# Kernel tuning notes

Measured on AMD Instinct MI355X. Metric: run time of the kernel, lower is better.

Reference implementation:

```python
import jax, jax.numpy as jnp
import numpy as np

EMBED = 512
OUT_DIM = 512
BS = 512


def _linear(x, W, b):
    return x @ W + b


def setup_inputs() -> dict:
    key = jax.random.key(0)
    ks = jax.random.split(key, 12)
    s = 1.0 / np.sqrt(EMBED)
    inp = {
        "image_features": jax.random.normal(ks[0], (BS, EMBED), jnp.float32),
        "text_features": jax.random.normal(ks[1], (BS, EMBED), jnp.float32),
        "cell_id": 1,
        # fusion weights (stored [in, out])
        "Wx": jax.random.uniform(ks[2], (EMBED, EMBED), jnp.float32, -s, s),
        "bx": jax.random.uniform(ks[3], (EMBED,), jnp.float32, -s, s),
        "Wy": jax.random.uniform(ks[4], (EMBED, EMBED), jnp.float32, -s, s),
        "by": jax.random.uniform(ks[5], (EMBED,), jnp.float32, -s, s),
        "Wo": jax.random.uniform(ks[6], (EMBED, OUT_DIM), jnp.float32, -s, s),
        "bo": jax.random.uniform(ks[7], (OUT_DIM,), jnp.float32, -s, s),
        # attention MLP weights
        "Wa1": jax.random.uniform(ks[8], (EMBED, EMBED), jnp.float32, -s, s),
        "ba1": jax.random.uniform(ks[9], (EMBED,), jnp.float32, -s, s),
        "Wa2": jax.random.uniform(ks[10], (EMBED, EMBED), jnp.float32, -s, s),
        "ba2": jax.random.uniform(ks[11], (EMBED,), jnp.float32, -s, s),
    }
    return inp


def reference(image_features, text_features, cell_id, Wx, bx, Wy, by, Wo, bo, Wa1, ba1, Wa2, ba2):
    # AttentionMechanism: Linear -> ReLU -> Linear -> Softmax over feature dim (dim=1)
    h = jax.nn.relu(_linear(text_features, Wa1, ba1))
    attn = jax.nn.softmax(_linear(h, Wa2, ba2), axis=1)
    text = attn * text_features  # [bs, d]

    out_x = _linear(image_features, Wx, bx)          # [bs, d]
    gate = jax.nn.sigmoid(_linear(text, Wy, by))     # [bs, d]

    if cell_id != 0 and cell_id != 3:
        # outs[i, j] = fc_out(gate[i] * out_x[j])  -> [bs, bs, out_dim]
        prod = gate[:, None, :] * out_x[None, :, :]  # [bs, bs, d]
        return jnp.einsum('ijd,do->ijo', prod, Wo) + bo
    else:
        return _linear(gate * out_x, Wo, bo)
```

## Files before the change

kernel.cpp:

```cpp
#include <hip/hip_runtime.h>
#include <hip/hip_bf16.h>

typedef __attribute__((ext_vector_type(4))) float f32x4;
typedef __attribute__((ext_vector_type(8))) __bf16 bf16x8;

__device__ __forceinline__ void gld_lds16(const void* g, void* l) {
  __builtin_amdgcn_global_load_lds((__attribute__((address_space(1))) void*)(g),
                                   (__attribute__((address_space(3))) void*)(l),
                                   16, 0, 0);
}

__device__ __forceinline__ f32x4 mfma16(bf16x8 a, bf16x8 b, f32x4 c) {
  return __builtin_amdgcn_mfma_f32_16x16x32_bf16(a, b, c, 0, 0, 0);
}

__device__ __forceinline__ bf16x8 cvt8(f32x4 a, f32x4 b) {
  bf16x8 r;
  r[0] = (__bf16)a.x; r[1] = (__bf16)a.y; r[2] = (__bf16)a.z; r[3] = (__bf16)a.w;
  r[4] = (__bf16)b.x; r[5] = (__bf16)b.y; r[6] = (__bf16)b.z; r[7] = (__bf16)b.w;
  return r;
}

__device__ __forceinline__ bf16x8 mulcvt8(f32x4 a, f32x4 b, f32x4 g0, f32x4 g1) {
  bf16x8 r;
  r[0] = (__bf16)(a.x * g0.x); r[1] = (__bf16)(a.y * g0.y);
  r[2] = (__bf16)(a.z * g0.z); r[3] = (__bf16)(a.w * g0.w);
  r[4] = (__bf16)(b.x * g1.x); r[5] = (__bf16)(b.y * g1.y);
  r[6] = (__bf16)(b.z * g1.z); r[7] = (__bf16)(b.w * g1.w);
  return r;
}

struct P5 {
  const float* s[5];
  __bf16* d[5];
};

__global__ __launch_bounds__(256) void transpose_cvt_k(P5 p) {
  __shared__ __bf16 tile[64][66];
  const float* src = p.s[blockIdx.z];
  __bf16* dst = p.d[blockIdx.z];
  const int x = threadIdx.x & 63, y = threadIdx.x >> 6;
  const int n0 = blockIdx.x * 64, k0 = blockIdx.y * 64;
#pragma unroll
  for (int r = 0; r < 16; ++r) {
    int k = r * 4 + y;
    tile[k][x] = (__bf16)src[(size_t)(k0 + k) * 512 + n0 + x];
  }
  __syncthreads();
#pragma unroll
  for (int r = 0; r < 16; ++r) {
    int n = r * 4 + y;
    dst[(size_t)(n0 + n) * 512 + k0 + x] = tile[x][n];
  }
}

template <int ACT>
__global__ __launch_bounds__(256) void gemm512(const float* __restrict__ A,
                                               const __bf16* __restrict__ Bt,
                                               const float* __restrict__ bias,
                                               float* __restrict__ C) {
  __shared__ alignas(16) __bf16 Als[64 * 32];
  __shared__ alignas(16) __bf16 Bls[64 * 32];
  const int t = threadIdx.x;
  const int w = t >> 6, L = t & 63, lq = L >> 4, l16 = L & 15;
  const int m0 = (blockIdx.x & 7) * 64, n0 = (blockIdx.x >> 3) * 64;
  const int wm = (w & 1) * 32, wn = (w >> 1) * 32;
  const int row = t >> 2, p = t & 3;
  const int q = p ^ ((row >> 1) & 3);

  const float* ap = A + (size_t)(m0 + row) * 512 + q * 8;
  const __bf16* bp = Bt + (size_t)(n0 + row) * 512 + q * 8;
  __bf16* aw = &Als[row * 32 + p * 8];
  void* bl = (void*)&Bls[w * 512];
  const int sq8 = (lq ^ ((l16 >> 1) & 3)) * 8;

  const f32x4 fz = {0.f, 0.f, 0.f, 0.f};
  f32x4 acc[2][2] = {{fz, fz}, {fz, fz}};

  for (int kt = 0; kt < 16; ++kt) {
    const int k0 = kt * 32;
    if (kt) __syncthreads();
    f32x4 a0 = *(const f32x4*)(ap + k0);
    f32x4 a1 = *(const f32x4*)(ap + k0 + 4);
    *(bf16x8*)aw = cvt8(a0, a1);
    gld_lds16(bp + k0, bl);
    __syncthreads();
    bf16x8 af[2], bb[2];
#pragma unroll
    for (int mt = 0; mt < 2; ++mt)
      af[mt] = *(const bf16x8*)&Als[(wm + mt * 16 + l16) * 32 + sq8];
#pragma unroll
    for (int nt = 0; nt < 2; ++nt)
      bb[nt] = *(const bf16x8*)&Bls[(wn + nt * 16 + l16) * 32 + sq8];
#pragma unroll
    for (int mt = 0; mt < 2; ++mt)
#pragma unroll
      for (int nt = 0; nt < 2; ++nt)
        acc[mt][nt] = mfma16(af[mt], bb[nt], acc[mt][nt]);
  }

#pragma unroll
  for (int nt = 0; nt < 2; ++nt) {
    const int o = n0 + wn + nt * 16 + l16;
    const float bv = bias[o];
#pragma unroll
    for (int mt = 0; mt < 2; ++mt) {
      const int mb = m0 + wm + mt * 16 + lq * 4;
#pragma unroll
      for (int r = 0; r < 4; ++r) {
        float v = acc[mt][nt][r] + bv;
        if (ACT == 1) v = fmaxf(v, 0.f);
        if (ACT == 2) v = 1.0f / (1.0f + __expf(-v));
        C[(size_t)(mb + r) * 512 + o] = v;
      }
    }
  }
}

__global__ __launch_bounds__(256) void softmax_mul_k(const float* __restrict__ S,
                                                     const float* __restrict__ T,
                                                     float* __restrict__ O) {
  const int i = blockIdx.x, t = threadIdx.x, w = t >> 6, L = t & 63;
  __shared__ float red[8];
  float v0 = S[i * 512 + t];
  float v1 = S[i * 512 + 256 + t];
  float m = fmaxf(v0, v1);
  for (int off = 32; off; off >>= 1) m = fmaxf(m, __shfl_xor(m, off));
  if (L == 0) red[w] = m;
  __syncthreads();
  m = fmaxf(fmaxf(red[0], red[1]), fmaxf(red[2], red[3]));
  float e0 = __expf(v0 - m), e1 = __expf(v1 - m);
  float sm = e0 + e1;
  for (int off = 32; off; off >>= 1) sm += __shfl_xor(sm, off);
  if (L == 0) red[4 + w] = sm;
  __syncthreads();
  sm = (red[4] + red[5]) + (red[6] + red[7]);
  const float inv = 1.0f / sm;
  O[i * 512 + t] = e0 * inv * T[i * 512 + t];
  O[i * 512 + 256 + t] = e1 * inv * T[i * 512 + 256 + t];
}

__global__ __launch_bounds__(256, 3) void einsum_main(
    const float* __restrict__ OX, const float* __restrict__ GATE,
    const __bf16* __restrict__ WOT, const float* __restrict__ BO,
    float* __restrict__ OUT) {
  __shared__ alignas(16) __bf16 Als[128 * 32];
  __shared__ alignas(16) __bf16 Bls[128 * 32];
  const int t = threadIdx.x;
  const int bx = blockIdx.x;
  const int i = bx >> 4;
  const int j0 = ((bx >> 2) & 3) * 128;
  const int o0 = (bx & 3) * 128;
  const int w = t >> 6, L = t & 63, lq = L >> 4, l16 = L & 15;
  const int wm = (w & 1) * 64, wn = (w >> 1) * 64;
  const int r0 = t >> 2, p = t & 3;
  const int q = p ^ ((r0 >> 1) & 3);

  const float* ox0 = OX + (size_t)(j0 + r0) * 512 + q * 8;
  const float* ox1 = ox0 + (size_t)64 * 512;
  const float* gp = GATE + (size_t)i * 512 + q * 8;
  const __bf16* wo0 = WOT + (size_t)(o0 + r0) * 512 + q * 8;
  const __bf16* wo1 = wo0 + (size_t)64 * 512;
  __bf16* aw0 = &Als[r0 * 32 + p * 8];
  __bf16* aw1 = &Als[(r0 + 64) * 32 + p * 8];
  void* bl0 = (void*)&Bls[w * 512];
  void* bl1 = (void*)&Bls[(w + 4) * 512];
  const int sq8 = (lq ^ ((l16 >> 1) & 3)) * 8;

  const f32x4 fz = {0.f, 0.f, 0.f, 0.f};
  f32x4 acc[4][4];
#pragma unroll
  for (int a = 0; a < 4; ++a)
#pragma unroll
    for (int b = 0; b < 4; ++b) acc[a][b] = fz;

  f32x4 xa0 = *(const f32x4*)ox0, xa1 = *(const f32x4*)(ox0 + 4);
  f32x4 xb0 = *(const f32x4*)ox1, xb1 = *(const f32x4*)(ox1 + 4);
  f32x4 g0 = *(const f32x4*)gp, g1 = *(const f32x4*)(gp + 4);

  for (int kt = 0; kt < 16; ++kt) {
    const int k0 = kt * 32;
    if (kt) __syncthreads();
    *(bf16x8*)aw0 = mulcvt8(xa0, xa1, g0, g1);
    *(bf16x8*)aw1 = mulcvt8(xb0, xb1, g0, g1);
    gld_lds16(wo0 + k0, bl0);
    gld_lds16(wo1 + k0, bl1);
    __syncthreads();
    if (kt < 15) {
      xa0 = *(const f32x4*)(ox0 + k0 + 32);
      xa1 = *(const f32x4*)(ox0 + k0 + 36);
      xb0 = *(const f32x4*)(ox1 + k0 + 32);
      xb1 = *(const f32x4*)(ox1 + k0 + 36);
      g0 = *(const f32x4*)(gp + k0 + 32);
      g1 = *(const f32x4*)(gp + k0 + 36);
    }
    bf16x8 af[4], bb[4];
#pragma unroll
    for (int mt = 0; mt < 4; ++mt)
      af[mt] = *(const bf16x8*)&Als[(wm + mt * 16 + l16) * 32 + sq8];
#pragma unroll
    for (int nt = 0; nt < 4; ++nt)
      bb[nt] = *(const bf16x8*)&Bls[(wn + nt * 16 + l16) * 32 + sq8];
#pragma unroll
    for (int mt = 0; mt < 4; ++mt)
#pragma unroll
      for (int nt = 0; nt < 4; ++nt)
        acc[mt][nt] = mfma16(af[mt], bb[nt], acc[mt][nt]);
  }

  const size_t obase = (size_t)i * 512 * 512;
#pragma unroll
  for (int nt = 0; nt < 4; ++nt) {
    const int o = o0 + wn + nt * 16 + l16;
    const float bv = BO[o];
#pragma unroll
    for (int mt = 0; mt < 4; ++mt) {
      const int jb = j0 + wm + mt * 16 + lq * 4;
#pragma unroll
      for (int r = 0; r < 4; ++r)
        OUT[obase + (size_t)(jb + r) * 512 + o] = acc[mt][nt][r] + bv;
    }
  }
}

extern "C" void kernel_launch(void* const* d_in, const int* in_sizes, int n_in,
                              void* d_out, int out_size, void* d_ws, size_t ws_size,
                              hipStream_t stream) {
  (void)in_sizes; (void)n_in; (void)out_size; (void)ws_size;
  const float* image = (const float*)d_in[0];
  const float* text  = (const float*)d_in[1];
  const float* Wx  = (const float*)d_in[3];
  const float* bx  = (const float*)d_in[4];
  const float* Wy  = (const float*)d_in[5];
  const float* by  = (const float*)d_in[6];
  const float* Wo  = (const float*)d_in[7];
  const float* bo  = (const float*)d_in[8];
  const float* Wa1 = (const float*)d_in[9];
  const float* ba1 = (const float*)d_in[10];
  const float* Wa2 = (const float*)d_in[11];
  const float* ba2 = (const float*)d_in[12];

  char* ws = (char*)d_ws;
  const size_t HB = 512 * 1024;
  const size_t FB = 1024 * 1024;
  __bf16* tWx  = (__bf16*)(ws + 0 * HB);
  __bf16* tWy  = (__bf16*)(ws + 1 * HB);
  __bf16* tWo  = (__bf16*)(ws + 2 * HB);
  __bf16* tWa1 = (__bf16*)(ws + 3 * HB);
  __bf16* tWa2 = (__bf16*)(ws + 4 * HB);
  char* fb = ws + 5 * HB;
  float* hbuf  = (float*)(fb + 0 * FB);
  float* sbuf  = (float*)(fb + 1 * FB);
  float* t2    = (float*)(fb + 2 * FB);
  float* oxb   = (float*)(fb + 3 * FB);
  float* gateb = (float*)(fb + 4 * FB);

  P5 p;
  p.s[0] = Wx;  p.d[0] = tWx;
  p.s[1] = Wy;  p.d[1] = tWy;
  p.s[2] = Wo;  p.d[2] = tWo;
  p.s[3] = Wa1; p.d[3] = tWa1;
  p.s[4] = Wa2; p.d[4] = tWa2;
  transpose_cvt_k<<<dim3(8, 8, 5), 256, 0, stream>>>(p);

  gemm512<1><<<64, 256, 0, stream>>>(text, tWa1, ba1, hbuf);
  gemm512<0><<<64, 256, 0, stream>>>(hbuf, tWa2, ba2, sbuf);
  softmax_mul_k<<<512, 256, 0, stream>>>(sbuf, text, t2);
  gemm512<0><<<64, 256, 0, stream>>>(image, tWx, bx, oxb);
  gemm512<2><<<64, 256, 0, stream>>>(t2, tWy, by, gateb);
  einsum_main<<<8192, 256, 0, stream>>>(oxb, gateb, tWo, bo, (float*)d_out);
}
```

Before: 728.7 us.

## Materialize gated bf16 products and batch independent small GEMMs

Independent GEMMs (Wa1 and Wx) are merged into one launch via blockIdx.y. If the workspace is large enough, the einsum no longer does an on-the-fly multiply and convert. A prescale kernel instead writes the full 512x512x512 bf16 gate*out_x tensor (256 MB), and a plain GEMM then streams it into LDS with direct global-to-LDS loads, using a swizzled block order. This trades the in-loop conversion work for a large extra memory write and read, and it only runs when ws_size allows.

```diff
diff --git a/kernel.cpp b/kernel.cpp
--- a/kernel.cpp
+++ b/kernel.cpp
@@ -54,16 +54,25 @@
   }
 }
 
-template <int ACT>
-__global__ __launch_bounds__(256) void gemm512(const float* __restrict__ A,
-                                               const __bf16* __restrict__ Bt,
-                                               const float* __restrict__ bias,
-                                               float* __restrict__ C) {
+struct GemmArgs {
+  const float* A;
+  const __bf16* Bt;
+  const float* bias;
+  float* C;
+  int act;
+};
+struct GemmPair { GemmArgs g[2]; };
+
+__device__ __forceinline__ void gemm512_body(const float* __restrict__ A,
+                                             const __bf16* __restrict__ Bt,
+                                             const float* __restrict__ bias,
+                                             float* __restrict__ C, int act,
+                                             int bidx) {
   __shared__ alignas(16) __bf16 Als[64 * 32];
   __shared__ alignas(16) __bf16 Bls[64 * 32];
   const int t = threadIdx.x;
   const int w = t >> 6, L = t & 63, lq = L >> 4, l16 = L & 15;
-  const int m0 = (blockIdx.x & 7) * 64, n0 = (blockIdx.x >> 3) * 64;
+  const int m0 = (bidx & 7) * 64, n0 = (bidx >> 3) * 64;
   const int wm = (w & 1) * 32, wn = (w >> 1) * 32;
   const int row = t >> 2, p = t & 3;
   const int q = p ^ ((row >> 1) & 3);
@@ -109,12 +118,21 @@
 #pragma unroll
       for (int r = 0; r < 4; ++r) {
         float v = acc[mt][nt][r] + bv;
-        if (ACT == 1) v = fmaxf(v, 0.f);
-        if (ACT == 2) v = 1.0f / (1.0f + __expf(-v));
+        if (act == 1) v = fmaxf(v, 0.f);
+        else if (act == 2) v = 1.0f / (1.0f + __expf(-v));
         C[(size_t)(mb + r) * 512 + o] = v;
       }
     }
   }
+}
+
+__global__ __launch_bounds__(256) void gemm512_one(GemmArgs a) {
+  gemm512_body(a.A, a.Bt, a.bias, a.C, a.act, blockIdx.x);
+}
+
+__global__ __launch_bounds__(256) void gemm512_two(GemmPair p) {
+  GemmArgs a = p.g[blockIdx.y];
+  gemm512_body(a.A, a.Bt, a.bias, a.C, a.act, blockIdx.x);
 }
 
 __global__ __launch_bounds__(256) void softmax_mul_k(const float* __restrict__ S,
@@ -140,6 +158,90 @@
   O[i * 512 + 256 + t] = e1 * inv * T[i * 512 + 256 + t];
 }
 
+__global__ __launch_bounds__(256) void prescale_k(const float* __restrict__ OX,
+                                                  const float* __restrict__ GATE,
+                                                  __bf16* __restrict__ A) {
+  const int total = 512 * 512 * 64;
+  const int stride = gridDim.x * 256;
+  for (int c = blockIdx.x * 256 + threadIdx.x; c < total; c += stride) {
+    const int d8 = c & 63, j = (c >> 6) & 511, i = c >> 15;
+    const float* ox = OX + j * 512 + d8 * 8;
+    const float* gp = GATE + i * 512 + d8 * 8;
+    f32x4 x0 = *(const f32x4*)ox, x1 = *(const f32x4*)(ox + 4);
+    f32x4 g0 = *(const f32x4*)gp, g1 = *(const f32x4*)(gp + 4);
+    *(bf16x8*)(A + (size_t)c * 8) = mulcvt8(x0, x1, g0, g1);
+  }
+}
+
+__global__ __launch_bounds__(256, 3) void einsum_gemm(
+    const __bf16* __restrict__ Aall, const __bf16* __restrict__ WOT,
+    const float* __restrict__ BO, float* __restrict__ OUT) {
+  __shared__ alignas(16) __bf16 Als[128 * 32];
+  __shared__ alignas(16) __bf16 Bls[128 * 32];
+  const int t = threadIdx.x;
+  const int bx = (blockIdx.x & 7) * 1024 + (blockIdx.x >> 3);
+  const int i = bx >> 4;
+  const int j0 = ((bx >> 2) & 3) * 128;
+  const int o0 = (bx & 3) * 128;
+  const int w = t >> 6, L = t & 63, lq = L >> 4, l16 = L & 15;
+  const int wm = (w & 1) * 64, wn = (w >> 1) * 64;
+  const int r0 = t >> 2, p = t & 3;
+  const int q = p ^ ((r0 >> 1) & 3);
+
+  const __bf16* a0 = Aall + ((size_t)i * 512 + j0 + r0) * 512 + q * 8;
+  const __bf16* a1 = a0 + (size_t)64 * 512;
+  const __bf16* b0 = WOT + (size_t)(o0 + r0) * 512 + q * 8;
+  const __bf16* b1 = b0 + (size_t)64 * 512;
+  void* al0 = (void*)&Als[w * 512];
+  void* al1 = (void*)&Als[(w + 4) * 512];
+  void* bl0 = (void*)&Bls[w * 512];
+  void* bl1 = (void*)&Bls[(w + 4) * 512];
+  const int sq8 = (lq ^ ((l16 >> 1) & 3)) * 8;
+
+  const f32x4 fz = {0.f, 0.f, 0.f, 0.f};
+  f32x4 acc[4][4];
+#pragma unroll
+  for (int a = 0; a < 4; ++a)
+#pragma unroll
+    for (int b = 0; b < 4; ++b) acc[a][b] = fz;
+
+  for (int kt = 0; kt < 16; ++kt) {
+    const int k0 = kt * 32;
+    if (kt) __syncthreads();
+    gld_lds16(a0 + k0, al0);
+    gld_lds16(a1 + k0, al1);
+    gld_lds16(b0 + k0, bl0);
+    gld_lds16(b1 + k0, bl1);
+    __syncthreads();
+    bf16x8 af[4], bb[4];
+#pragma unroll
+    for (int mt = 0; mt < 4; ++mt)
+      af[mt] = *(const bf16x8*)&Als[(wm + mt * 16 + l16) * 32 + sq8];
+#pragma unroll
+    for (int nt = 0; nt < 4; ++nt)
+      bb[nt] = *(const bf16x8*)&Bls[(wn + nt * 16 + l16) * 32 + sq8];
+#pragma unroll
+    for (int mt = 0; mt < 4; ++mt)
+#pragma unroll
+      for (int nt = 0; nt < 4; ++nt)
+        acc[mt][nt] = mfma16(af[mt], bb[nt], acc[mt][nt]);
+  }
+
+  const size_t obase = (size_t)i * 512 * 512;
+#pragma unroll
+  for (int nt = 0; nt < 4; ++nt) {
+    const int o = o0 + wn + nt * 16 + l16;
+    const float bv = BO[o];
+#pragma unroll
+    for (int mt = 0; mt < 4; ++mt) {
+      const int jb = j0 + wm + mt * 16 + lq * 4;
+#pragma unroll
+      for (int r = 0; r < 4; ++r)
+        OUT[obase + (size_t)(jb + r) * 512 + o] = acc[mt][nt][r] + bv;
+    }
+  }
+}
+
 __global__ __launch_bounds__(256, 3) void einsum_main(
     const float* __restrict__ OX, const float* __restrict__ GATE,
     const __bf16* __restrict__ WOT, const float* __restrict__ BO,
@@ -226,7 +328,7 @@
 extern "C" void kernel_launch(void* const* d_in, const int* in_sizes, int n_in,
                               void* d_out, int out_size, void* d_ws, size_t ws_size,
                               hipStream_t stream) {
-  (void)in_sizes; (void)n_in; (void)out_size; (void)ws_size;
+  (void)in_sizes; (void)n_in; (void)out_size;
   const float* image = (const float*)d_in[0];
   const float* text  = (const float*)d_in[1];
   const float* Wx  = (const float*)d_in[3];
@@ -254,6 +356,9 @@
   float* t2    = (float*)(fb + 2 * FB);
   float* oxb   = (float*)(fb + 3 * FB);
   float* gateb = (float*)(fb + 4 * FB);
+  __bf16* Aall = (__bf16*)(fb + 5 * FB);
+  const size_t need_big =
+      5 * HB + 5 * FB + (size_t)512 * 512 * 512 * 2;
 
   P5 p;
   p.s[0] = Wx;  p.d[0] = tWx;
@@ -263,10 +368,18 @@
   p.s[4] = Wa2; p.d[4] = tWa2;
   transpose_cvt_k<<<dim3(8, 8, 5), 256, 0, stream>>>(p);
 
-  gemm512<1><<<64, 256, 0, stream>>>(text, tWa1, ba1, hbuf);
-  gemm512<0><<<64, 256, 0, stream>>>(hbuf, tWa2, ba2, sbuf);
+  GemmPair pp;
+  pp.g[0] = GemmArgs{text, tWa1, ba1, hbuf, 1};
+  pp.g[1] = GemmArgs{image, tWx, bx, oxb, 0};
+  gemm512_two<<<dim3(64, 2), 256, 0, stream>>>(pp);
+  gemm512_one<<<64, 256, 0, stream>>>(GemmArgs{hbuf, tWa2, ba2, sbuf, 0});
   softmax_mul_k<<<512, 256, 0, stream>>>(sbuf, text, t2);
-  gemm512<0><<<64, 256, 0, stream>>>(image, tWx, bx, oxb);
-  gemm512<2><<<64, 256, 0, stream>>>(t2, tWy, by, gateb);
-  einsum_main<<<8192, 256, 0, stream>>>(oxb, gateb, tWo, bo, (float*)d_out);
-}
+  gemm512_one<<<64, 256, 0, stream>>>(GemmArgs{t2, tWy, by, gateb, 2});
+
+  if (ws_size >= need_big) {
+    prescale_k<<<4096, 256, 0, stream>>>(oxb, gateb, Aall);
+    einsum_gemm<<<8192, 256, 0, stream>>>(Aall, tWo, bo, (float*)d_out);
+  } else {
+    einsum_main<<<8192, 256, 0, stream>>>(oxb, gateb, tWo, bo, (float*)d_out);
+  }
+}
```

Result: slower. 785.3 us (+7.8%).

## Rework einsum kernel tiling with K=64 stages, 8 waves, and vectorized stores

Applied to the files above, without the earlier changes.

The main einsum kernel now runs 512 threads (8 waves) per 128x128 tile with a 64-wide K step and an XOR swizzle over 8 chunks. It swaps the MFMA operand order so each lane holds 4 consecutive output columns and can write them with one float4 store. The image projection GEMM is also batched into one launch with the first attention GEMM to cut launch count. The aim is fewer barriers, wider coalesced writes of the large output, and better latency hiding, at the cost of more LDS per block and lower per-wave reuse.

```diff
diff --git a/kernel.cpp b/kernel.cpp
--- a/kernel.cpp
+++ b/kernel.cpp
@@ -54,16 +54,25 @@
   }
 }
 
-template <int ACT>
-__global__ __launch_bounds__(256) void gemm512(const float* __restrict__ A,
-                                               const __bf16* __restrict__ Bt,
-                                               const float* __restrict__ bias,
-                                               float* __restrict__ C) {
+struct GemmArgs {
+  const float* A;
+  const __bf16* Bt;
+  const float* bias;
+  float* C;
+  int act;
+};
+struct GemmPair { GemmArgs g[2]; };
+
+__device__ __forceinline__ void gemm512_body(const float* __restrict__ A,
+                                             const __bf16* __restrict__ Bt,
+                                             const float* __restrict__ bias,
+                                             float* __restrict__ C, int act,
+                                             int bidx) {
   __shared__ alignas(16) __bf16 Als[64 * 32];
   __shared__ alignas(16) __bf16 Bls[64 * 32];
   const int t = threadIdx.x;
   const int w = t >> 6, L = t & 63, lq = L >> 4, l16 = L & 15;
-  const int m0 = (blockIdx.x & 7) * 64, n0 = (blockIdx.x >> 3) * 64;
+  const int m0 = (bidx & 7) * 64, n0 = (bidx >> 3) * 64;
   const int wm = (w & 1) * 32, wn = (w >> 1) * 32;
   const int row = t >> 2, p = t & 3;
   const int q = p ^ ((row >> 1) & 3);
@@ -109,12 +118,21 @@
 #pragma unroll
       for (int r = 0; r < 4; ++r) {
         float v = acc[mt][nt][r] + bv;
-        if (ACT == 1) v = fmaxf(v, 0.f);
-        if (ACT == 2) v = 1.0f / (1.0f + __expf(-v));
+        if (act == 1) v = fmaxf(v, 0.f);
+        else if (act == 2) v = 1.0f / (1.0f + __expf(-v));
         C[(size_t)(mb + r) * 512 + o] = v;
       }
     }
   }
+}
+
+__global__ __launch_bounds__(256) void gemm512_one(GemmArgs a) {
+  gemm512_body(a.A, a.Bt, a.bias, a.C, a.act, blockIdx.x);
+}
+
+__global__ __launch_bounds__(256) void gemm512_two(GemmPair p) {
+  GemmArgs a = p.g[blockIdx.y];
+  gemm512_body(a.A, a.Bt, a.bias, a.C, a.act, blockIdx.x);
 }
 
 __global__ __launch_bounds__(256) void softmax_mul_k(const float* __restrict__ S,
@@ -140,85 +158,110 @@
   O[i * 512 + 256 + t] = e1 * inv * T[i * 512 + 256 + t];
 }
 
-__global__ __launch_bounds__(256, 3) void einsum_main(
+__global__ __launch_bounds__(512, 4) void einsum_v2(
     const float* __restrict__ OX, const float* __restrict__ GATE,
     const __bf16* __restrict__ WOT, const float* __restrict__ BO,
     float* __restrict__ OUT) {
-  __shared__ alignas(16) __bf16 Als[128 * 32];
-  __shared__ alignas(16) __bf16 Bls[128 * 32];
+  __shared__ alignas(16) __bf16 Als[128 * 64];
+  __shared__ alignas(16) __bf16 Bls[128 * 64];
   const int t = threadIdx.x;
   const int bx = blockIdx.x;
   const int i = bx >> 4;
   const int j0 = ((bx >> 2) & 3) * 128;
   const int o0 = (bx & 3) * 128;
   const int w = t >> 6, L = t & 63, lq = L >> 4, l16 = L & 15;
-  const int wm = (w & 1) * 64, wn = (w >> 1) * 64;
-  const int r0 = t >> 2, p = t & 3;
-  const int q = p ^ ((r0 >> 1) & 3);
-
-  const float* ox0 = OX + (size_t)(j0 + r0) * 512 + q * 8;
-  const float* ox1 = ox0 + (size_t)64 * 512;
-  const float* gp = GATE + (size_t)i * 512 + q * 8;
-  const __bf16* wo0 = WOT + (size_t)(o0 + r0) * 512 + q * 8;
-  const __bf16* wo1 = wo0 + (size_t)64 * 512;
-  __bf16* aw0 = &Als[r0 * 32 + p * 8];
-  __bf16* aw1 = &Als[(r0 + 64) * 32 + p * 8];
+  const int wj = (w & 1) * 64;
+  const int wo = (w >> 1) * 32;
+
+  const int rA = t >> 2;
+  const int lc0 = (t & 3) * 2, lc1 = lc0 + 1;
+  __bf16* aw0 = &Als[rA * 64 + ((lc0 ^ (rA & 7)) * 8)];
+  __bf16* aw1 = &Als[rA * 64 + ((lc1 ^ (rA & 7)) * 8)];
+  const float* oxp = OX + (size_t)(j0 + rA) * 512;
+  const float* gp = GATE + (size_t)i * 512;
+  const int oo0 = lc0 * 8, oo1 = lc1 * 8;
+
+  const int rB = t >> 3;
+  const int qB = (t & 7) ^ (rB & 7);
+  const __bf16* bsrc0 = WOT + (size_t)(o0 + rB) * 512 + qB * 8;
+  const __bf16* bsrc1 = WOT + (size_t)(o0 + 64 + rB) * 512 + qB * 8;
   void* bl0 = (void*)&Bls[w * 512];
-  void* bl1 = (void*)&Bls[(w + 4) * 512];
-  const int sq8 = (lq ^ ((l16 >> 1) & 3)) * 8;
+  void* bl1 = (void*)&Bls[4096 + w * 512];
+
+  const int cx0 = ((lq ^ (l16 & 7)) * 8);
+  const int cx1 = (((4 + lq) ^ (l16 & 7)) * 8);
+  const int arow = (wj + l16) * 64;
+  const int brow = (wo + l16) * 64;
 
   const f32x4 fz = {0.f, 0.f, 0.f, 0.f};
-  f32x4 acc[4][4];
+  f32x4 acc[4][2];
 #pragma unroll
   for (int a = 0; a < 4; ++a)
 #pragma unroll
-    for (int b = 0; b < 4; ++b) acc[a][b] = fz;
-
-  f32x4 xa0 = *(const f32x4*)ox0, xa1 = *(const f32x4*)(ox0 + 4);
-  f32x4 xb0 = *(const f32x4*)ox1, xb1 = *(const f32x4*)(ox1 + 4);
-  f32x4 g0 = *(const f32x4*)gp, g1 = *(const f32x4*)(gp + 4);
-
-  for (int kt = 0; kt < 16; ++kt) {
-    const int k0 = kt * 32;
+    for (int b = 0; b < 2; ++b) acc[a][b] = fz;
+
+  f32x4 x0a = *(const f32x4*)(oxp + oo0);
+  f32x4 x0b = *(const f32x4*)(oxp + oo0 + 4);
+  f32x4 x1a = *(const f32x4*)(oxp + oo1);
+  f32x4 x1b = *(const f32x4*)(oxp + oo1 + 4);
+  f32x4 g0a = *(const f32x4*)(gp + oo0);
+  f32x4 g0b = *(const f32x4*)(gp + oo0 + 4);
+  f32x4 g1a = *(const f32x4*)(gp + oo1);
+  f32x4 g1b = *(const f32x4*)(gp + oo1 + 4);
+
+  for (int kt = 0; kt < 8; ++kt) {
+    const int k0 = kt * 64;
     if (kt) __syncthreads();
-    *(bf16x8*)aw0 = mulcvt8(xa0, xa1, g0, g1);
-    *(bf16x8*)aw1 = mulcvt8(xb0, xb1, g0, g1);
-    gld_lds16(wo0 + k0, bl0);
-    gld_lds16(wo1 + k0, bl1);
+    *(bf16x8*)aw0 = mulcvt8(x0a, x0b, g0a, g0b);
+    *(bf16x8*)aw1 = mulcvt8(x1a, x1b, g1a, g1b);
+    gld_lds16(bsrc0 + k0, bl0);
+    gld_lds16(bsrc1 + k0, bl1);
     __syncthreads();
-    if (kt < 15) {
-      xa0 = *(const f32x4*)(ox0 + k0 + 32);
-      xa1 = *(const f32x4*)(ox0 + k0 + 36);
-      xb0 = *(const f32x4*)(ox1 + k0 + 32);
-      xb1 = *(const f32x4*)(ox1 + k0 + 36);
-      g0 = *(const f32x4*)(gp + k0 + 32);
-      g1 = *(const f32x4*)(gp + k0 + 36);
+    if (kt < 7) {
+      x0a = *(const f32x4*)(oxp + k0 + 64 + oo0);
+      x0b = *(const f32x4*)(oxp + k0 + 64 + oo0 + 4);
+      x1a = *(const f32x4*)(oxp + k0 + 64 + oo1);
+      x1b = *(const f32x4*)(oxp + k0 + 64 + oo1 + 4);
+      g0a = *(const f32x4*)(gp + k0 + 64 + oo0);
+      g0b = *(const f32x4*)(gp + k0 + 64 + oo0 + 4);
+      g1a = *(const f32x4*)(gp + k0 + 64 + oo1);
+      g1b = *(const f32x4*)(gp + k0 + 64 + oo1 + 4);
     }
-    bf16x8 af[4], bb[4];
+    bf16x8 af[4], bb[2];
 #pragma unroll
     for (int mt = 0; mt < 4; ++mt)
-      af[mt] = *(const bf16x8*)&Als[(wm + mt * 16 + l16) * 32 + sq8];
-#pragma unroll
-    for (int nt = 0; nt < 4; ++nt)
-      bb[nt] = *(const bf16x8*)&Bls[(wn + nt * 16 + l16) * 32 + sq8];
+      af[mt] = *(const bf16x8*)&Als[arow + mt * 1024 + cx0];
+#pragma unroll
+    for (int nt = 0; nt < 2; ++nt)
+      bb[nt] = *(const bf16x8*)&Bls[brow + nt * 1024 + cx0];
 #pragma unroll
     for (int mt = 0; mt < 4; ++mt)
 #pragma unroll
-      for (int nt = 0; nt < 4; ++nt)
-        acc[mt][nt] = mfma16(af[mt], bb[nt], acc[mt][nt]);
+      for (int nt = 0; nt < 2; ++nt)
+        acc[mt][nt] = mfma16(bb[nt], af[mt], acc[mt][nt]);
+#pragma unroll
+    for (int mt = 0; mt < 4; ++mt)
+      af[mt] = *(const bf16x8*)&Als[arow + mt * 1024 + cx1];
+#pragma unroll
+    for (int nt = 0; nt < 2; ++nt)
+      bb[nt] = *(const bf16x8*)&Bls[brow + nt * 1024 + cx1];
+#pragma unroll
+    for (int mt = 0; mt < 4; ++mt)
+#pragma unroll
+      for (int nt = 0; nt < 2; ++nt)
+        acc[mt][nt] = mfma16(bb[nt], af[mt], acc[mt][nt]);
   }
 
   const size_t obase = (size_t)i * 512 * 512;
 #pragma unroll
-  for (int nt = 0; nt < 4; ++nt) {
-    const int o = o0 + wn + nt * 16 + l16;
-    const float bv = BO[o];
+  for (int nt = 0; nt < 2; ++nt) {
+    const int ob = o0 + wo + nt * 16 + lq * 4;
+    const f32x4 bo4 = *(const f32x4*)(BO + ob);
 #pragma unroll
     for (int mt = 0; mt < 4; ++mt) {
-      const int jb = j0 + wm + mt * 16 + lq * 4;
-#pragma unroll
-      for (int r = 0; r < 4; ++r)
-        OUT[obase + (size_t)(jb + r) * 512 + o] = acc[mt][nt][r] + bv;
+      const int j = j0 + wj + mt * 16 + l16;
+      f32x4 v = acc[mt][nt] + bo4;
+      *(f32x4*)(OUT + obase + (size_t)j * 512 + ob) = v;
     }
   }
 }
@@ -263,10 +306,12 @@
   p.s[4] = Wa2; p.d[4] = tWa2;
   transpose_cvt_k<<<dim3(8, 8, 5), 256, 0, stream>>>(p);
 
-  gemm512<1><<<64, 256, 0, stream>>>(text, tWa1, ba1, hbuf);
-  gemm512<0><<<64, 256, 0, stream>>>(hbuf, tWa2, ba2, sbuf);
+  GemmPair pp;
+  pp.g[0] = GemmArgs{text, tWa1, ba1, hbuf, 1};
+  pp.g[1] = GemmArgs{image, tWx, bx, oxb, 0};
+  gemm512_two<<<dim3(64, 2), 256, 0, stream>>>(pp);
+  gemm512_one<<<64, 256, 0, stream>>>(GemmArgs{hbuf, tWa2, ba2, sbuf, 0});
   softmax_mul_k<<<512, 256, 0, stream>>>(sbuf, text, t2);
-  gemm512<0><<<64, 256, 0, stream>>>(image, tWx, bx, oxb);
-  gemm512<2><<<64, 256, 0, stream>>>(t2, tWy, by, gateb);
-  einsum_main<<<8192, 256, 0, stream>>>(oxb, gateb, tWo, bo, (float*)d_out);
-}
+  gemm512_one<<<64, 256, 0, stream>>>(GemmArgs{t2, tWy, by, gateb, 2});
+  einsum_v2<<<8192, 512, 0, stream>>>(oxb, gateb, tWo, bo, (float*)d_out);
+}
```

Measured after the change: 846.1 us. +16.1%, slower.

## Double-buffer einsum LDS tiles, loop 4 gate rows per block, batch independent GEMMs

Applied to the files above, without the earlier changes.

The main einsum kernel now double-buffers its A and B tiles in LDS and prefetches the next two stages into registers. This leaves one barrier per k-step and overlaps loads with MFMA work. Each block now handles 4 consecutive i rows, reusing the same OX/Wo tile indices, which cuts the grid from 8192 to 2048 blocks. The two independent small GEMMs (Wa1 and Wx) are merged into one launch via blockIdx.y, trading compile-time activation templates for a runtime flag. Doubling LDS use may lower occupancy.

```diff
diff --git a/kernel.cpp b/kernel.cpp
--- a/kernel.cpp
+++ b/kernel.cpp
@@ -54,16 +54,25 @@
   }
 }
 
-template <int ACT>
-__global__ __launch_bounds__(256) void gemm512(const float* __restrict__ A,
-                                               const __bf16* __restrict__ Bt,
-                                               const float* __restrict__ bias,
-                                               float* __restrict__ C) {
+struct GemmArgs {
+  const float* A;
+  const __bf16* Bt;
+  const float* bias;
+  float* C;
+  int act;
+};
+struct GemmPair { GemmArgs g[2]; };
+
+__device__ __forceinline__ void gemm512_body(const float* __restrict__ A,
+                                             const __bf16* __restrict__ Bt,
+                                             const float* __restrict__ bias,
+                                             float* __restrict__ C, int act,
+                                             int bidx) {
   __shared__ alignas(16) __bf16 Als[64 * 32];
   __shared__ alignas(16) __bf16 Bls[64 * 32];
   const int t = threadIdx.x;
   const int w = t >> 6, L = t & 63, lq = L >> 4, l16 = L & 15;
-  const int m0 = (blockIdx.x & 7) * 64, n0 = (blockIdx.x >> 3) * 64;
+  const int m0 = (bidx & 7) * 64, n0 = (bidx >> 3) * 64;
   const int wm = (w & 1) * 32, wn = (w >> 1) * 32;
   const int row = t >> 2, p = t & 3;
   const int q = p ^ ((row >> 1) & 3);
@@ -109,12 +118,21 @@
 #pragma unroll
       for (int r = 0; r < 4; ++r) {
         float v = acc[mt][nt][r] + bv;
-        if (ACT == 1) v = fmaxf(v, 0.f);
-        if (ACT == 2) v = 1.0f / (1.0f + __expf(-v));
+        if (act == 1) v = fmaxf(v, 0.f);
+        else if (act == 2) v = 1.0f / (1.0f + __expf(-v));
         C[(size_t)(mb + r) * 512 + o] = v;
       }
     }
   }
+}
+
+__global__ __launch_bounds__(256) void gemm512_one(GemmArgs a) {
+  gemm512_body(a.A, a.Bt, a.bias, a.C, a.act, blockIdx.x);
+}
+
+__global__ __launch_bounds__(256) void gemm512_two(GemmPair p) {
+  GemmArgs a = p.g[blockIdx.y];
+  gemm512_body(a.A, a.Bt, a.bias, a.C, a.act, blockIdx.x);
 }
 
 __global__ __launch_bounds__(256) void softmax_mul_k(const float* __restrict__ S,
@@ -140,15 +158,28 @@
   O[i * 512 + 256 + t] = e1 * inv * T[i * 512 + 256 + t];
 }
 
-__global__ __launch_bounds__(256, 3) void einsum_main(
+struct AStage {
+  f32x4 xa0, xa1, xb0, xb1, g0, g1;
+};
+
+__device__ __forceinline__ AStage load_stage(const float* ox0, const float* ox1,
+                                             const float* gp, int k0) {
+  AStage s;
+  s.xa0 = *(const f32x4*)(ox0 + k0); s.xa1 = *(const f32x4*)(ox0 + k0 + 4);
+  s.xb0 = *(const f32x4*)(ox1 + k0); s.xb1 = *(const f32x4*)(ox1 + k0 + 4);
+  s.g0  = *(const f32x4*)(gp + k0);  s.g1  = *(const f32x4*)(gp + k0 + 4);
+  return s;
+}
+
+__global__ __launch_bounds__(256, 3) void einsum_v3(
     const float* __restrict__ OX, const float* __restrict__ GATE,
     const __bf16* __restrict__ WOT, const float* __restrict__ BO,
     float* __restrict__ OUT) {
-  __shared__ alignas(16) __bf16 Als[128 * 32];
-  __shared__ alignas(16) __bf16 Bls[128 * 32];
+  __shared__ alignas(16) __bf16 Als[2][128 * 32];
+  __shared__ alignas(16) __bf16 Bls[2][128 * 32];
   const int t = threadIdx.x;
   const int bx = blockIdx.x;
-  const int i = bx >> 4;
+  const int i0 = (bx >> 4) * 4;
   const int j0 = ((bx >> 2) & 3) * 128;
   const int o0 = (bx & 3) * 128;
   const int w = t >> 6, L = t & 63, lq = L >> 4, l16 = L & 15;
@@ -158,67 +189,70 @@
 
   const float* ox0 = OX + (size_t)(j0 + r0) * 512 + q * 8;
   const float* ox1 = ox0 + (size_t)64 * 512;
-  const float* gp = GATE + (size_t)i * 512 + q * 8;
   const __bf16* wo0 = WOT + (size_t)(o0 + r0) * 512 + q * 8;
   const __bf16* wo1 = wo0 + (size_t)64 * 512;
-  __bf16* aw0 = &Als[r0 * 32 + p * 8];
-  __bf16* aw1 = &Als[(r0 + 64) * 32 + p * 8];
-  void* bl0 = (void*)&Bls[w * 512];
-  void* bl1 = (void*)&Bls[(w + 4) * 512];
+  const int awo = r0 * 32 + p * 8;
   const int sq8 = (lq ^ ((l16 >> 1) & 3)) * 8;
 
-  const f32x4 fz = {0.f, 0.f, 0.f, 0.f};
-  f32x4 acc[4][4];
-#pragma unroll
-  for (int a = 0; a < 4; ++a)
-#pragma unroll
-    for (int b = 0; b < 4; ++b) acc[a][b] = fz;
-
-  f32x4 xa0 = *(const f32x4*)ox0, xa1 = *(const f32x4*)(ox0 + 4);
-  f32x4 xb0 = *(const f32x4*)ox1, xb1 = *(const f32x4*)(ox1 + 4);
-  f32x4 g0 = *(const f32x4*)gp, g1 = *(const f32x4*)(gp + 4);
-
-  for (int kt = 0; kt < 16; ++kt) {
-    const int k0 = kt * 32;
-    if (kt) __syncthreads();
-    *(bf16x8*)aw0 = mulcvt8(xa0, xa1, g0, g1);
-    *(bf16x8*)aw1 = mulcvt8(xb0, xb1, g0, g1);
-    gld_lds16(wo0 + k0, bl0);
-    gld_lds16(wo1 + k0, bl1);
+  for (int g = 0; g < 4; ++g) {
+    const float* gp = GATE + (size_t)(i0 + g) * 512 + q * 8;
+
+    const f32x4 fz = {0.f, 0.f, 0.f, 0.f};
+    f32x4 acc[4][4];
+#pragma unroll
+    for (int a = 0; a < 4; ++a)
+#pragma unroll
+      for (int b = 0; b < 4; ++b) acc[a][b] = fz;
+
+    AStage S[2];
+    S[0] = load_stage(ox0, ox1, gp, 0);
+    *(bf16x8*)&Als[0][awo] = mulcvt8(S[0].xa0, S[0].xa1, S[0].g0, S[0].g1);
+    *(bf16x8*)&Als[0][awo + 64 * 32] =
+        mulcvt8(S[0].xb0, S[0].xb1, S[0].g0, S[0].g1);
+    gld_lds16(wo0, (void*)&Bls[0][w * 512]);
+    gld_lds16(wo1, (void*)&Bls[0][(w + 4) * 512]);
+    S[1] = load_stage(ox0, ox1, gp, 32);
     __syncthreads();
-    if (kt < 15) {
-      xa0 = *(const f32x4*)(ox0 + k0 + 32);
-      xa1 = *(const f32x4*)(ox0 + k0 + 36);
-      xb0 = *(const f32x4*)(ox1 + k0 + 32);
-      xb1 = *(const f32x4*)(ox1 + k0 + 36);
-      g0 = *(const f32x4*)(gp + k0 + 32);
-      g1 = *(const f32x4*)(gp + k0 + 36);
+
+#pragma unroll
+    for (int kt = 0; kt < 16; ++kt) {
+      const int cb = kt & 1, nb = cb ^ 1;
+      if (kt < 15) {
+        *(bf16x8*)&Als[nb][awo] =
+            mulcvt8(S[nb].xa0, S[nb].xa1, S[nb].g0, S[nb].g1);
+        *(bf16x8*)&Als[nb][awo + 64 * 32] =
+            mulcvt8(S[nb].xb0, S[nb].xb1, S[nb].g0, S[nb].g1);
+        gld_lds16(wo0 + (kt + 1) * 32, (void*)&Bls[nb][w * 512]);
+        gld_lds16(wo1 + (kt + 1) * 32, (void*)&Bls[nb][(w + 4) * 512]);
+      }
+      if (kt < 14) S[cb] = load_stage(ox0, ox1, gp, (kt + 2) * 32);
+      bf16x8 af[4], bb[4];
+#pragma unroll
+      for (int mt = 0; mt < 4; ++mt)
+        af[mt] = *(const bf16x8*)&Als[cb][(wm + mt * 16 + l16) * 32 + sq8];
+#pragma unroll
+      for (int nt = 0; nt < 4; ++nt)
+        bb[nt] = *(const bf16x8*)&Bls[cb][(wn + nt * 16 + l16) * 32 + sq8];
+#pragma unroll
+      for (int mt = 0; mt < 4; ++mt)
+#pragma unroll
+        for (int nt = 0; nt < 4; ++nt)
+          acc[mt][nt] = mfma16(af[mt], bb[nt], acc[mt][nt]);
+      __syncthreads();
     }
-    bf16x8 af[4], bb[4];
-#pragma unroll
-    for (int mt = 0; mt < 4; ++mt)
-      af[mt] = *(const bf16x8*)&Als[(wm + mt * 16 + l16) * 32 + sq8];
-#pragma unroll
-    for (int nt = 0; nt < 4; ++nt)
-      bb[nt] = *(const bf16x8*)&Bls[(wn + nt * 16 + l16) * 32 + sq8];
-#pragma unroll
-    for (int mt = 0; mt < 4; ++mt)
-#pragma unroll
-      for (int nt = 0; nt < 4; ++nt)
-        acc[mt][nt] = mfma16(af[mt], bb[nt], acc[mt][nt]);
-  }
-
-  const size_t obase = (size_t)i * 512 * 512;
-#pragma unroll
-  for (int nt = 0; nt < 4; ++nt) {
-    const int o = o0 + wn + nt * 16 + l16;
-    const float bv = BO[o];
-#pragma unroll
-    for (int mt = 0; mt < 4; ++mt) {
-      const int jb = j0 + wm + mt * 16 + lq * 4;
-#pragma unroll
-      for (int r = 0; r < 4; ++r)
-        OUT[obase + (size_t)(jb + r) * 512 + o] = acc[mt][nt][r] + bv;
+
+    const size_t obase = (size_t)(i0 + g) * 512 * 512;
+#pragma unroll
+    for (int nt = 0; nt < 4; ++nt) {
+      const int o = o0 + wn + nt * 16 + l16;
+      const float bv = BO[o];
+#pragma unroll
+      for (int mt = 0; mt < 4; ++mt) {
+        const int jb = j0 + wm + mt * 16 + lq * 4;
+#pragma unroll
+        for (int r = 0; r < 4; ++r)
+          OUT[obase + (size_t)(jb + r) * 512 + o] = acc[mt][nt][r] + bv;
+      }
     }
   }
 }
@@ -263,10 +297,12 @@
   p.s[4] = Wa2; p.d[4] = tWa2;
   transpose_cvt_k<<<dim3(8, 8, 5), 256, 0, stream>>>(p);
 
-  gemm512<1><<<64, 256, 0, stream>>>(text, tWa1, ba1, hbuf);
-  gemm512<0><<<64, 256, 0, stream>>>(hbuf, tWa2, ba2, sbuf);
+  GemmPair pp;
+  pp.g[0] = GemmArgs{text, tWa1, ba1, hbuf, 1};
+  pp.g[1] = GemmArgs{image, tWx, bx, oxb, 0};
+  gemm512_two<<<dim3(64, 2), 256, 0, stream>>>(pp);
+  gemm512_one<<<64, 256, 0, stream>>>(GemmArgs{hbuf, tWa2, ba2, sbuf, 0});
   softmax_mul_k<<<512, 256, 0, stream>>>(sbuf, text, t2);
-  gemm512<0><<<64, 256, 0, stream>>>(image, tWx, bx, oxb);
-  gemm512<2><<<64, 256, 0, stream>>>(t2, tWy, by, gateb);
-  einsum_main<<<8192, 256, 0, stream>>>(oxb, gateb, tWo, bo, (float*)d_out);
-}
+  gemm512_one<<<64, 256, 0, stream>>>(GemmArgs{t2, tWy, by, gateb, 2});
+  einsum_v3<<<2048, 256, 0, stream>>>(oxb, gateb, tWo, bo, (float*)d_out);
+}
```

New measurement: 1.652 ms. +126.7%, slower.
